# Optimization experiments

Hardware: AMD Instinct MI355X
Metric: run time of the kernel (lower is better)

The kernel has to match this reference:

```python
import jax, jax.numpy as jnp
import numpy as np

C = 512
GROUPS = 8
EPS = 1e-5


def setup_inputs() -> dict:
    key = jax.random.key(0)
    ks = jax.random.split(key, 7)
    B, H, W = 16, 32, 32
    x = jax.random.normal(ks[0], (B, C, H, W), dtype=jnp.float32)
    gn_w = jnp.ones((C,), jnp.float32)
    gn_b = jnp.zeros((C,), jnp.float32)
    s = 1.0 / np.sqrt(C)
    qkv_w = jax.random.normal(ks[1], (3 * C, C), dtype=jnp.float32) * s
    qkv_b = jnp.zeros((3 * C,), jnp.float32)
    proj_w = jax.random.normal(ks[2], (C, C), dtype=jnp.float32) * s
    proj_b = jnp.zeros((C,), jnp.float32)
    return {"x": x, "gn_w": gn_w, "gn_b": gn_b, "qkv_w": qkv_w,
            "qkv_b": qkv_b, "proj_w": proj_w, "proj_b": proj_b}


def _group_norm(x, w, b):
    B, Cc, H, W = x.shape
    xg = x.reshape(B, GROUPS, Cc // GROUPS, H, W)
    mean = xg.mean(axis=(2, 3, 4), keepdims=True)
    var = xg.var(axis=(2, 3, 4), keepdims=True)
    xn = ((xg - mean) * jax.lax.rsqrt(var + EPS)).reshape(B, Cc, H, W)
    return xn * w[None, :, None, None] + b[None, :, None, None]


def reference(x, gn_w, gn_b, qkv_w, qkv_b, proj_w, proj_b):
    B, Cc, H, W = x.shape
    N = H * W
    h = _group_norm(x, gn_w, gn_b)
    # 1x1 conv == per-pixel matmul over channels
    qkv = jnp.einsum('bchw,oc->bohw', h, qkv_w) + qkv_b[None, :, None, None]
    q, k, v = jnp.split(qkv, 3, axis=1)          # each (B, C, H, W)
    q = q.reshape(B, Cc, N).transpose(0, 2, 1)   # (B, N, C)
    k = k.reshape(B, Cc, N)                      # (B, C, N)
    v = v.reshape(B, Cc, N).transpose(0, 2, 1)   # (B, N, C)
    attn = jnp.einsum('bnc,bcm->bnm', q, k) * (Cc ** -0.5)
    attn = jax.nn.softmax(attn, axis=-1)
    h = jnp.einsum('bnm,bmc->bnc', attn, v)      # (B, N, C)
    h = h.transpose(0, 2, 1).reshape(B, Cc, H, W)
    out = jnp.einsum('bchw,oc->bohw', h, proj_w) + proj_b[None, :, None, None]
    return x + out
```

## Files before the change

kernel.cpp:

```cpp
#include <hip/hip_runtime.h>


typedef __bf16 bf16x8 __attribute__((ext_vector_type(8)));
typedef float f32x4 __attribute__((ext_vector_type(4)));
typedef unsigned short u16x8 __attribute__((ext_vector_type(8)));
typedef unsigned short u16x4 __attribute__((ext_vector_type(4)));

#define DEVINL __device__ __forceinline__

DEVINL float b2f(unsigned short u) {
  unsigned int x = ((unsigned int)u) << 16;
  return __builtin_bit_cast(float, x);
}
DEVINL unsigned short f2b(float f) {
  unsigned int x = __builtin_bit_cast(unsigned int, f);
  x += 0x7fffu + ((x >> 16) & 1u);
  return (unsigned short)(x >> 16);
}

DEVINL void gload16(const void* g, void* l) {
  __builtin_amdgcn_global_load_lds(
      (const __attribute__((address_space(1))) unsigned int*)(const void*)g,
      (__attribute__((address_space(3))) unsigned int*)l, 16, 0, 0);
}

__global__ __launch_bounds__(256)
void f2bf_all(const float* __restrict__ qw, const float* __restrict__ pw,
              unsigned short* __restrict__ wq, unsigned short* __restrict__ wp) {
  const int i = blockIdx.x * 256 + threadIdx.x;
  const bool isq = i < 196608;
  const int j = isq ? i : i - 196608;
  float4 v = isq ? ((const float4*)qw)[j] : ((const float4*)pw)[j];
  u16x4 o;
  o[0] = f2b(v.x); o[1] = f2b(v.y); o[2] = f2b(v.z); o[3] = f2b(v.w);
  if (isq) ((u16x4*)wq)[j] = o; else ((u16x4*)wp)[j] = o;
}

__global__ __launch_bounds__(512)
void gn_fused(const float* __restrict__ x, const float* __restrict__ gw,
              const float* __restrict__ gb, unsigned short* __restrict__ h) {
  const int b = blockIdx.x >> 3, g = blockIdx.x & 7;
  const float* base = x + (long long)(b * 512 + g * 64) * 1024;
  float s = 0.f, q = 0.f;
  for (int i = threadIdx.x; i < 16384; i += 512) {
    float4 v = ((const float4*)base)[i];
    s += v.x + v.y + v.z + v.w;
    q += v.x * v.x + v.y * v.y + v.z * v.z + v.w * v.w;
  }
#pragma unroll
  for (int off = 32; off; off >>= 1) { s += __shfl_xor(s, off); q += __shfl_xor(q, off); }
  __shared__ float ss[8], qs[8], stats[2];
  const int wave = threadIdx.x >> 6, lane = threadIdx.x & 63;
  if (lane == 0) { ss[wave] = s; qs[wave] = q; }
  __syncthreads();
  if (threadIdx.x == 0) {
    float S = 0.f, Q = 0.f;
#pragma unroll
    for (int w = 0; w < 8; ++w) { S += ss[w]; Q += qs[w]; }
    float mu = S * (1.f / 65536.f);
    float var = Q * (1.f / 65536.f) - mu * mu;
    stats[0] = mu;
    stats[1] = rsqrtf(var + 1e-5f);
  }
  __syncthreads();
  const float mu = stats[0], rs = stats[1];
  __shared__ float t[64][65];
  const int r8 = threadIdx.x >> 6, cl = threadIdx.x & 63;
  for (int pt = 0; pt < 16; ++pt) {
    const int p0 = pt << 6;
#pragma unroll
    for (int i = 0; i < 8; ++i) {
      int c = i * 8 + r8;
      float v = base[(long long)c * 1024 + p0 + cl];
      t[c][cl] = (v - mu) * rs * gw[g * 64 + c] + gb[g * 64 + c];
    }
    __syncthreads();
#pragma unroll
    for (int i = 0; i < 8; ++i) {
      int pr = i * 8 + r8;
      h[(long long)(b * 1024 + p0 + pr) * 512 + g * 64 + cl] = f2b(t[cl][pr]);
    }
    __syncthreads();
  }
}

__global__ __launch_bounds__(256)
void softmax_rows(unsigned short* __restrict__ S) {
  const long long row = (long long)blockIdx.x * 4 + (threadIdx.x >> 6);
  const int lane = threadIdx.x & 63;
  u16x8* p = (u16x8*)(S + row * 1024);
  u16x8 a = p[lane], b = p[64 + lane];
  float v[16];
#pragma unroll
  for (int i = 0; i < 8; ++i) { v[i] = b2f(a[i]); v[8 + i] = b2f(b[i]); }
  float m = v[0];
#pragma unroll
  for (int i = 1; i < 16; ++i) m = fmaxf(m, v[i]);
#pragma unroll
  for (int off = 32; off; off >>= 1) m = fmaxf(m, __shfl_xor(m, off));
  float s = 0.f;
#pragma unroll
  for (int i = 0; i < 16; ++i) { v[i] = __expf(v[i] - m); s += v[i]; }
#pragma unroll
  for (int off = 32; off; off >>= 1) s += __shfl_xor(s, off);
  float inv = 1.f / s;
#pragma unroll
  for (int i = 0; i < 8; ++i) { a[i] = f2b(v[i] * inv); b[i] = f2b(v[8 + i] * inv); }
  p[lane] = a;
  p[64 + lane] = b;
}

#define RSQRT_C 0.044194173824159216f
enum { EPI_BF16 = 0, EPI_QKV = 1, EPI_PROJ = 2 };

DEVINL void stage_tile(const unsigned short* __restrict__ Ab,
                       const unsigned short* __restrict__ Bb,
                       int lda, int ldb, int k0, char* lb, int tid, int wave) {
#pragma unroll
  for (int i = 0; i < 4; ++i) {
    const int c = (i << 8) + tid;
    const int r = c >> 3;
    const int sk = ((c & 7) ^ (r & 7)) << 3;
    char* la = lb + (((i << 8) + (wave << 6)) << 4);
    gload16(Ab + (long long)r * lda + k0 + sk, la);
    gload16(Bb + (long long)r * ldb + k0 + sk, la + 16384);
  }
}

template <int EPI>
__global__ __launch_bounds__(256, 2)
void gemm_bt(const unsigned short* __restrict__ A, int lda, long long sA,
             const unsigned short* __restrict__ B, int ldb, long long sB,
             void* __restrict__ Cv, int ldc, long long sC, int K,
             const float* __restrict__ bias, const float* __restrict__ resid,
             unsigned short* __restrict__ aux, int gx, int gy) {
  __shared__ char lds[65536];
  const int tid = threadIdx.x;
  const int wave = tid >> 6, lane = tid & 63;
  const int wr = wave >> 1, wc = wave & 1;

  const int nwg = gridDim.x;
  const int id0 = blockIdx.x;
  const int id = (id0 & 7) * (nwg >> 3) + (id0 >> 3);
  const int bn = id % gx;
  const int t1 = id / gx;
  const int bm = t1 % gy;
  const int bz = t1 / gy;

  const unsigned short* Ab = A + (long long)bz * sA + (long long)bm * 128 * lda;
  const unsigned short* Bb = B + (long long)bz * sB + (long long)bn * 128 * ldb;

  f32x4 acc[4][4] = {};
  const int frow = lane & 15;
  const int fkb = (lane >> 4) << 4;
  const int swr = (frow & 7) << 4;
  const int NT = K >> 6;

  stage_tile(Ab, Bb, lda, ldb, 0, lds, tid, wave);
  stage_tile(Ab, Bb, lda, ldb, 64, lds + 32768, tid, wave);
  asm volatile("s_waitcnt vmcnt(8)" ::: "memory");

  for (int kt = 0; kt < NT; ++kt) {
    const int cur = kt & 1;
    __builtin_amdgcn_s_barrier();
    asm volatile("" ::: "memory");
    const char* lb = lds + cur * 32768;
    __builtin_amdgcn_s_setprio(1);
#pragma unroll
    for (int ks = 0; ks < 2; ++ks) {
      bf16x8 af[4], bfr[4];
      const int kb = (ks << 6) + fkb;
#pragma unroll
      for (int f = 0; f < 4; ++f) {
        const int ar = (wr << 6) + (f << 4) + frow;
        af[f] = *reinterpret_cast<const bf16x8*>(lb + ar * 128 + (kb ^ swr));
        const int br = (wc << 6) + (f << 4) + frow;
        bfr[f] = *reinterpret_cast<const bf16x8*>(lb + 16384 + br * 128 + (kb ^ swr));
      }
#pragma unroll
      for (int i = 0; i < 4; ++i)
#pragma unroll
        for (int j = 0; j < 4; ++j)
          acc[i][j] = __builtin_amdgcn_mfma_f32_16x16x32_bf16(af[i], bfr[j], acc[i][j], 0, 0, 0);
    }
    __builtin_amdgcn_s_setprio(0);
    asm volatile("" ::: "memory");
    __builtin_amdgcn_s_barrier();
    if (kt + 2 < NT) {
      stage_tile(Ab, Bb, lda, ldb, (kt + 2) << 6, lds + cur * 32768, tid, wave);
      asm volatile("s_waitcnt vmcnt(8)" ::: "memory");
    } else if (kt + 2 == NT) {
      asm volatile("s_waitcnt vmcnt(0)" ::: "memory");
    }
  }

  const int rb = bm * 128 + (wr << 6) + ((lane >> 4) << 2);
  const int cb = bn * 128 + (wc << 6) + (lane & 15);
#pragma unroll
  for (int i = 0; i < 4; ++i) {
#pragma unroll
    for (int j = 0; j < 4; ++j) {
      const int col = cb + (j << 4);
      if constexpr (EPI == EPI_QKV) {
        if (col >= 1024) {
          const int row0 = rb + (i << 4);
          const int bb = row0 >> 10, p0 = row0 & 1023;
          u16x4 o;
#pragma unroll
          for (int r = 0; r < 4; ++r) o[r] = f2b(acc[i][j][r] + bias[col]);
          *(u16x4*)(aux + (long long)bb * 524288 + (long long)(col - 1024) * 1024 + p0) = o;
          continue;
        }
      }
#pragma unroll
      for (int r = 0; r < 4; ++r) {
        const int row = rb + (i << 4) + r;
        float v = acc[i][j][r];
        if constexpr (EPI == EPI_BF16) {
          ((unsigned short*)Cv)[(long long)bz * sC + (long long)row * ldc + col] = f2b(v);
        } else if constexpr (EPI == EPI_QKV) {
          v += bias[col];
          if (col < 512) v *= RSQRT_C;
          ((unsigned short*)Cv)[(long long)row * ldc + col] = f2b(v);
        } else {
          long long idx = (long long)bz * sC + (long long)row * ldc + col;
          ((float*)Cv)[idx] = v + bias[row] + resid[idx];
        }
      }
    }
  }
}

extern "C" void kernel_launch(void* const* d_in, const int* in_sizes, int n_in,
                              void* d_out, int out_size, void* d_ws, size_t ws_size,
                              hipStream_t stream) {
  const float* x      = (const float*)d_in[0];
  const float* gn_w   = (const float*)d_in[1];
  const float* gn_b   = (const float*)d_in[2];
  const float* qkv_w  = (const float*)d_in[3];
  const float* qkv_b  = (const float*)d_in[4];
  const float* proj_w = (const float*)d_in[5];
  const float* proj_b = (const float*)d_in[6];

  char* ws = (char*)d_ws;
  unsigned short* wq   = (unsigned short*)(ws + 1024);
  unsigned short* wp   = (unsigned short*)(ws + 1573888);
  unsigned short* h    = (unsigned short*)(ws + 2098176);
  unsigned short* qkv  = (unsigned short*)(ws + 18875392);
  unsigned short* vt   = (unsigned short*)(ws + 52429824);
  unsigned short* O    = h;
  unsigned short* S    = (unsigned short*)d_out;

  f2bf_all<<<1024, 256, 0, stream>>>(qkv_w, proj_w, wq, wp);
  gn_fused<<<128, 512, 0, stream>>>(x, gn_w, gn_b, h);
  gemm_bt<EPI_QKV><<<1536, 256, 0, stream>>>(
      h, 512, 0, wq, 512, 0, qkv, 1024, 0, 512, qkv_b, nullptr, vt, 12, 128);
  gemm_bt<EPI_BF16><<<1024, 256, 0, stream>>>(
      qkv, 1024, 1024LL * 1024, qkv + 512, 1024, 1024LL * 1024,
      S, 1024, 1024LL * 1024, 512, nullptr, nullptr, nullptr, 8, 8);
  softmax_rows<<<4096, 256, 0, stream>>>(S);
  gemm_bt<EPI_BF16><<<512, 256, 0, stream>>>(
      S, 1024, 1024LL * 1024, vt, 1024, 512LL * 1024,
      O, 512, 1024LL * 512, 1024, nullptr, nullptr, nullptr, 4, 8);
  gemm_bt<EPI_PROJ><<<512, 256, 0, stream>>>(
      wp, 512, 0, O, 512, 1024LL * 512,
      d_out, 1024, 512LL * 1024, 512, proj_b, x, nullptr, 8, 4);
}
```

Baseline: 237.5 us.

## Use 256x256-tile 8-wave GEMM kernel for QKV and QK^T products

```diff
diff --git a/kernel.cpp b/kernel.cpp
--- a/kernel.cpp
+++ b/kernel.cpp
@@ -113,6 +113,164 @@
 #define RSQRT_C 0.044194173824159216f
 enum { EPI_BF16 = 0, EPI_QKV = 1, EPI_PROJ = 2 };
 
+template <int EPI>
+__global__ __launch_bounds__(512, 1)
+void gemm256(const unsigned short* __restrict__ A, int lda, long long sA,
+             const unsigned short* __restrict__ B, int ldb, long long sB,
+             void* __restrict__ Cv, int ldc, long long sC, int K,
+             const float* __restrict__ bias, unsigned short* __restrict__ aux,
+             int gx, int gy) {
+  extern __shared__ char lds[];
+  const int tid = threadIdx.x;
+  const int wave = tid >> 6, lane = tid & 63;
+  const int wr = wave >> 2, wc = wave & 3;
+
+  const int nwg = gridDim.x;
+  const int id0 = blockIdx.x;
+  const int id = (id0 & 7) * (nwg >> 3) + (id0 >> 3);
+  const int bn = id % gx;
+  const int t1 = id / gx;
+  const int bm = t1 % gy;
+  const int bz = t1 / gy;
+
+  const unsigned short* Ab = A + (long long)bz * sA + (long long)bm * 256 * lda;
+  const unsigned short* Bb = B + (long long)bz * sB + (long long)bn * 256 * ldb;
+
+  f32x4 acc[8][4] = {};
+  const int frow = lane & 15;
+  const int fkb = (lane >> 4) << 4;
+  const int swr = (frow & 7) << 4;
+  const int NT = K >> 6;
+
+  auto STAGE = [&](int kt, int u, int buf) {
+    const unsigned short* Ob = (u < 2) ? Ab : Bb;
+    const int ld = (u < 2) ? lda : ldb;
+    const int half = u & 1;
+    const int k0 = kt << 6;
+#pragma unroll
+    for (int i = 0; i < 2; ++i) {
+      const int c = tid + (i << 9);
+      const int r = c >> 3;
+      const int sk = ((c & 7) ^ (r & 7)) << 3;
+      char* la = lds + buf * 65536 + u * 16384 + (((i << 9) + (wave << 6)) << 4);
+      gload16(Ob + (long long)(half * 128 + r) * ld + k0 + sk, la);
+    }
+  };
+
+  STAGE(0, 0, 0); STAGE(0, 1, 0); STAGE(0, 2, 0); STAGE(0, 3, 0);
+  asm volatile("s_waitcnt vmcnt(0)" ::: "memory");
+  __builtin_amdgcn_s_barrier();
+
+  for (int T = 0; T < NT; ++T) {
+    const int cur = T & 1, nxt = cur ^ 1;
+    const char* laA = lds + cur * 65536 + wr * 16384;
+    const char* laB = lds + cur * 65536 + 32768 + (wc >> 1) * 16384;
+    const int brow = (wc & 1) << 6;
+    const bool pf = (T + 1 < NT);
+    bf16x8 fA[4], fB[4];
+
+    if (pf) { STAGE(T + 1, 0, nxt); STAGE(T + 1, 1, nxt); }
+#pragma unroll
+    for (int f = 0; f < 4; ++f) {
+      fA[f] = *(const bf16x8*)(laA + (f * 16 + frow) * 128 + (fkb ^ swr));
+      fB[f] = *(const bf16x8*)(laB + (brow + f * 16 + frow) * 128 + (fkb ^ swr));
+    }
+    __builtin_amdgcn_s_barrier();
+    asm volatile("s_waitcnt lgkmcnt(0)" ::: "memory");
+    __builtin_amdgcn_sched_barrier(0);
+    __builtin_amdgcn_s_setprio(1);
+#pragma unroll
+    for (int mi = 0; mi < 4; ++mi)
+#pragma unroll
+      for (int nj = 0; nj < 4; ++nj)
+        acc[mi][nj] = __builtin_amdgcn_mfma_f32_16x16x32_bf16(fA[mi], fB[nj], acc[mi][nj], 0, 0, 0);
+    __builtin_amdgcn_s_setprio(0);
+    __builtin_amdgcn_s_barrier();
+
+    if (pf) { STAGE(T + 1, 2, nxt); STAGE(T + 1, 3, nxt); }
+#pragma unroll
+    for (int f = 0; f < 4; ++f)
+      fA[f] = *(const bf16x8*)(laA + ((f + 4) * 16 + frow) * 128 + (fkb ^ swr));
+    __builtin_amdgcn_s_barrier();
+    asm volatile("s_waitcnt lgkmcnt(0)" ::: "memory");
+    __builtin_amdgcn_sched_barrier(0);
+    __builtin_amdgcn_s_setprio(1);
+#pragma unroll
+    for (int mi = 0; mi < 4; ++mi)
+#pragma unroll
+      for (int nj = 0; nj < 4; ++nj)
+        acc[mi + 4][nj] = __builtin_amdgcn_mfma_f32_16x16x32_bf16(fA[mi], fB[nj], acc[mi + 4][nj], 0, 0, 0);
+    __builtin_amdgcn_s_setprio(0);
+    __builtin_amdgcn_s_barrier();
+
+#pragma unroll
+    for (int f = 0; f < 4; ++f) {
+      fA[f] = *(const bf16x8*)(laA + (f * 16 + frow) * 128 + ((64 + fkb) ^ swr));
+      fB[f] = *(const bf16x8*)(laB + (brow + f * 16 + frow) * 128 + ((64 + fkb) ^ swr));
+    }
+    __builtin_amdgcn_s_barrier();
+    asm volatile("s_waitcnt lgkmcnt(0)" ::: "memory");
+    __builtin_amdgcn_sched_barrier(0);
+    __builtin_amdgcn_s_setprio(1);
+#pragma unroll
+    for (int mi = 0; mi < 4; ++mi)
+#pragma unroll
+      for (int nj = 0; nj < 4; ++nj)
+        acc[mi][nj] = __builtin_amdgcn_mfma_f32_16x16x32_bf16(fA[mi], fB[nj], acc[mi][nj], 0, 0, 0);
+    __builtin_amdgcn_s_setprio(0);
+    __builtin_amdgcn_s_barrier();
+
+#pragma unroll
+    for (int f = 0; f < 4; ++f)
+      fA[f] = *(const bf16x8*)(laA + ((f + 4) * 16 + frow) * 128 + ((64 + fkb) ^ swr));
+    asm volatile("s_waitcnt vmcnt(0)" ::: "memory");
+    __builtin_amdgcn_s_barrier();
+    asm volatile("s_waitcnt lgkmcnt(0)" ::: "memory");
+    __builtin_amdgcn_sched_barrier(0);
+    __builtin_amdgcn_s_setprio(1);
+#pragma unroll
+    for (int mi = 0; mi < 4; ++mi)
+#pragma unroll
+      for (int nj = 0; nj < 4; ++nj)
+        acc[mi + 4][nj] = __builtin_amdgcn_mfma_f32_16x16x32_bf16(fA[mi], fB[nj], acc[mi + 4][nj], 0, 0, 0);
+    __builtin_amdgcn_s_setprio(0);
+    __builtin_amdgcn_s_barrier();
+  }
+
+  const int rb = bm * 256 + wr * 128 + ((lane >> 4) << 2);
+  const int cb = bn * 256 + wc * 64 + frow;
+#pragma unroll
+  for (int mi = 0; mi < 8; ++mi) {
+#pragma unroll
+    for (int nj = 0; nj < 4; ++nj) {
+      const int col = cb + nj * 16;
+      if constexpr (EPI == EPI_QKV) {
+        if (col >= 1024) {
+          const int row0 = rb + mi * 16;
+          const int bb = row0 >> 10, p0 = row0 & 1023;
+          u16x4 o;
+#pragma unroll
+          for (int r = 0; r < 4; ++r) o[r] = f2b(acc[mi][nj][r] + bias[col]);
+          *(u16x4*)(aux + (long long)bb * 524288 + (long long)(col - 1024) * 1024 + p0) = o;
+          continue;
+        }
+      }
+#pragma unroll
+      for (int r = 0; r < 4; ++r) {
+        const int row = rb + mi * 16 + r;
+        float v = acc[mi][nj][r];
+        if constexpr (EPI == EPI_BF16) {
+          ((unsigned short*)Cv)[(long long)bz * sC + (long long)row * ldc + col] = f2b(v);
+        } else if constexpr (EPI == EPI_QKV) {
+          v += bias[col];
+          if (col < 512) v *= RSQRT_C;
+          ((unsigned short*)Cv)[(long long)row * ldc + col] = f2b(v);
+        }
+      }
+    }
+  }
+}
+
 DEVINL void stage_tile(const unsigned short* __restrict__ Ab,
                        const unsigned short* __restrict__ Bb,
                        int lda, int ldb, int k0, char* lb, int tid, int wave) {
@@ -133,7 +291,7 @@
              const unsigned short* __restrict__ B, int ldb, long long sB,
              void* __restrict__ Cv, int ldc, long long sC, int K,
              const float* __restrict__ bias, const float* __restrict__ resid,
-             unsigned short* __restrict__ aux, int gx, int gy) {
+             int gx, int gy) {
   __shared__ char lds[65536];
   const int tid = threadIdx.x;
   const int wave = tid >> 6, lane = tid & 63;
@@ -195,33 +353,18 @@
   }
 
   const int rb = bm * 128 + (wr << 6) + ((lane >> 4) << 2);
-  const int cb = bn * 128 + (wc << 6) + (lane & 15);
+  const int cb = bn * 128 + (wc << 6) + frow;
 #pragma unroll
   for (int i = 0; i < 4; ++i) {
 #pragma unroll
     for (int j = 0; j < 4; ++j) {
       const int col = cb + (j << 4);
-      if constexpr (EPI == EPI_QKV) {
-        if (col >= 1024) {
-          const int row0 = rb + (i << 4);
-          const int bb = row0 >> 10, p0 = row0 & 1023;
-          u16x4 o;
-#pragma unroll
-          for (int r = 0; r < 4; ++r) o[r] = f2b(acc[i][j][r] + bias[col]);
-          *(u16x4*)(aux + (long long)bb * 524288 + (long long)(col - 1024) * 1024 + p0) = o;
-          continue;
-        }
-      }
 #pragma unroll
       for (int r = 0; r < 4; ++r) {
         const int row = rb + (i << 4) + r;
         float v = acc[i][j][r];
         if constexpr (EPI == EPI_BF16) {
           ((unsigned short*)Cv)[(long long)bz * sC + (long long)row * ldc + col] = f2b(v);
-        } else if constexpr (EPI == EPI_QKV) {
-          v += bias[col];
-          if (col < 512) v *= RSQRT_C;
-          ((unsigned short*)Cv)[(long long)row * ldc + col] = f2b(v);
         } else {
           long long idx = (long long)bz * sC + (long long)row * ldc + col;
           ((float*)Cv)[idx] = v + bias[row] + resid[idx];
@@ -251,18 +394,23 @@
   unsigned short* O    = h;
   unsigned short* S    = (unsigned short*)d_out;
 
+  (void)hipFuncSetAttribute(reinterpret_cast<const void*>(&gemm256<EPI_QKV>),
+                            hipFuncAttributeMaxDynamicSharedMemorySize, 131072);
+  (void)hipFuncSetAttribute(reinterpret_cast<const void*>(&gemm256<EPI_BF16>),
+                            hipFuncAttributeMaxDynamicSharedMemorySize, 131072);
+
   f2bf_all<<<1024, 256, 0, stream>>>(qkv_w, proj_w, wq, wp);
   gn_fused<<<128, 512, 0, stream>>>(x, gn_w, gn_b, h);
-  gemm_bt<EPI_QKV><<<1536, 256, 0, stream>>>(
-      h, 512, 0, wq, 512, 0, qkv, 1024, 0, 512, qkv_b, nullptr, vt, 12, 128);
-  gemm_bt<EPI_BF16><<<1024, 256, 0, stream>>>(
+  gemm256<EPI_QKV><<<384, 512, 131072, stream>>>(
+      h, 512, 0, wq, 512, 0, qkv, 1024, 0, 512, qkv_b, vt, 6, 64);
+  gemm256<EPI_BF16><<<256, 512, 131072, stream>>>(
       qkv, 1024, 1024LL * 1024, qkv + 512, 1024, 1024LL * 1024,
-      S, 1024, 1024LL * 1024, 512, nullptr, nullptr, nullptr, 8, 8);
+      S, 1024, 1024LL * 1024, 512, nullptr, nullptr, 4, 4);
   softmax_rows<<<4096, 256, 0, stream>>>(S);
   gemm_bt<EPI_BF16><<<512, 256, 0, stream>>>(
       S, 1024, 1024LL * 1024, vt, 1024, 512LL * 1024,
-      O, 512, 1024LL * 512, 1024, nullptr, nullptr, nullptr, 4, 8);
+      O, 512, 1024LL * 512, 1024, nullptr, nullptr, 4, 8);
   gemm_bt<EPI_PROJ><<<512, 256, 0, stream>>>(
       wp, 512, 0, O, 512, 1024LL * 512,
-      d_out, 1024, 512LL * 1024, 512, proj_b, x, nullptr, 8, 4);
-}
+      d_out, 1024, 512LL * 1024, 512, proj_b, x, 8, 4);
+}
```

After: 246.1 us. 1.04x slower.
